# Performance work log

Measured on AMD Instinct MI355X. Metric: run time of the kernel, lower is better.

Reference implementation:

```python
import jax, jax.numpy as jnp
import numpy as np

N, E, FIN, H, C = 100000, 1600000, 128, 64, 40
EPS = 1e-5

def setup_inputs() -> dict:
    key = jax.random.key(0)
    ks = jax.random.split(key, 20)
    inp = {
        'x': jax.random.normal(ks[0], (N, FIN), jnp.float32),
        'edge_idx': jax.random.randint(ks[1], (2, E), 0, N, dtype=jnp.int64),
        'W1': jax.random.normal(ks[2], (FIN, H), jnp.float32) / np.sqrt(FIN),
        'b1': jnp.zeros((H,), jnp.float32),
        'g1': jnp.ones((H,), jnp.float32),
        'be1': jnp.zeros((H,), jnp.float32),
        'm1': jax.random.normal(ks[3], (H,), jnp.float32) * 0.1,
        'v1': jax.random.uniform(ks[4], (H,), jnp.float32) + 0.5,
        'W2': jax.random.normal(ks[5], (H, H), jnp.float32) / np.sqrt(H),
        'b2': jnp.zeros((H,), jnp.float32),
        'g2': jnp.ones((H,), jnp.float32),
        'be2': jnp.zeros((H,), jnp.float32),
        'm2': jax.random.normal(ks[6], (H,), jnp.float32) * 0.1,
        'v2': jax.random.uniform(ks[7], (H,), jnp.float32) + 0.5,
        'W3': jax.random.normal(ks[8], (H, C), jnp.float32) / np.sqrt(H),
        'b3': jnp.zeros((C,), jnp.float32),
    }
    return inp

def reference(x, edge_idx, W1, b1, g1, be1, m1, v1, W2, b2, g2, be2, m2, v2, W3, b3):
    n = x.shape[0]
    loop = jnp.arange(n, dtype=edge_idx.dtype)
    row = jnp.concatenate([edge_idx[0], loop])  # source nodes (+ self loops)
    col = jnp.concatenate([edge_idx[1], loop])  # target nodes (+ self loops)
    # symmetric gcn_norm: deg from unit edge weights aggregated at target
    deg = jax.ops.segment_sum(jnp.ones_like(row, dtype=x.dtype), col, num_segments=n)
    dinv = jnp.where(deg > 0, jax.lax.rsqrt(deg), 0.0)
    norm = dinv[row] * dinv[col]  # [E+N]

    def conv(h, W, b):
        hl = h @ W                            # dense transform first (PyG order)
        msg = hl[row] * norm[:, None]         # gather + edge scale
        agg = jax.ops.segment_sum(msg, col, num_segments=n)  # scatter-add
        return agg + b

    def bn(h, g, be, m, v):  # eval-mode BatchNorm1d (running stats)
        return g * (h - m) * jax.lax.rsqrt(v + EPS) + be

    h = jax.nn.relu(bn(conv(x, W1, b1), g1, be1, m1, v1))
    h = jax.nn.relu(bn(conv(h, W2, b2), g2, be2, m2, v2))
    return conv(h, W3, b3)
```

## Files before the change

### kernel.cpp

```cpp
#include <hip/hip_runtime.h>

#define EPSV 1e-5f
#define NB  1024
#define CAP 2048

typedef short short8 __attribute__((ext_vector_type(8)));
typedef float f32x4 __attribute__((ext_vector_type(4)));

__device__ inline unsigned short f2bf(float x) {
    unsigned u = __float_as_uint(x);
    unsigned r = (u + 0x7FFFu + ((u >> 16) & 1u)) >> 16;
    return (unsigned short)r;
}
__device__ inline float bf2f(unsigned short h) {
    return __uint_as_float(((unsigned)h) << 16);
}
__device__ inline float bflo(unsigned u) { return __uint_as_float(u << 16); }
__device__ inline float bfhi(unsigned u) { return __uint_as_float(u & 0xffff0000u); }
__device__ inline unsigned packbf(float x, float y) {
    return (unsigned)f2bf(x) | ((unsigned)f2bf(y) << 16);
}


__global__ __launch_bounds__(512) void k_bin(const int* __restrict__ row,
                                             const int* __restrict__ col,
                                             int* __restrict__ bcnt,
                                             unsigned* __restrict__ bkt,
                                             int E, int npb, int chunk) {
    __shared__ int hist[NB];
    __shared__ int fill[NB];
    const int tid = threadIdx.x;
    const int e0 = blockIdx.x * chunk;
    const int e1 = min(E, e0 + chunk);
    for (int j = tid; j < NB; j += 512) hist[j] = 0;
    __syncthreads();
    for (int i = e0 + tid; i < e1; i += 512)
        atomicAdd(&hist[col[i] / npb], 1);
    __syncthreads();
    for (int j = tid; j < NB; j += 512)
        fill[j] = hist[j] ? atomicAdd(&bcnt[j], hist[j]) : 0;
    __syncthreads();
    for (int i = e0 + tid; i < e1; i += 512) {
        const int c = col[i], r = row[i];
        const int b = c / npb;
        const int pos = atomicAdd(&fill[b], 1);
        if (pos < CAP)
            bkt[(size_t)b * CAP + pos] = ((unsigned)(c - b * npb) << 17) | (unsigned)r;
    }
}


__global__ __launch_bounds__(NB) void k_bscan(const int* __restrict__ bcnt,
                                              int* __restrict__ bbase,
                                              int* __restrict__ rowptr, int E, int n) {
    __shared__ int s[NB];
    const int t = threadIdx.x;
    const int v = min(bcnt[t], CAP);
    s[t] = v;
    __syncthreads();
    for (int off = 1; off < NB; off <<= 1) {
        int u = (t >= off) ? s[t - off] : 0;
        __syncthreads();
        s[t] += u;
        __syncthreads();
    }
    bbase[t] = s[t] - v;
    if (t == 0) rowptr[n] = E;
}


__global__ __launch_bounds__(256) void k_place(const int* __restrict__ bcnt,
                                               const int* __restrict__ bbase,
                                               const unsigned* __restrict__ bkt,
                                               int* __restrict__ rowptr,
                                               float* __restrict__ dinv,
                                               int* __restrict__ srcidx,
                                               int n, int npb) {
    __shared__ int hist[128];
    __shared__ int pfx[128];
    __shared__ unsigned ent[CAP];
    const int b = blockIdx.x;
    const int tid = threadIdx.x;
    const int c0 = b * npb;
    const int nn = min(npb, n - c0);
    if (nn <= 0) return;
    const int bc = min(bcnt[b], CAP);
    const int base = bbase[b];
    for (int j = tid; j < nn; j += 256) hist[j] = 0;
    __syncthreads();
    for (int i = tid; i < bc; i += 256) {
        const unsigned e = bkt[(size_t)b * CAP + i];
        ent[i] = e;
        atomicAdd(&hist[e >> 17], 1);
    }
    __syncthreads();
    if (tid == 0) {
        int run = base;
        for (int j = 0; j < nn; ++j) { pfx[j] = run; run += hist[j]; }
    }
    __syncthreads();
    for (int j = tid; j < nn; j += 256) {
        rowptr[c0 + j] = pfx[j];
        dinv[c0 + j] = rsqrtf((float)(hist[j] + 1));
    }
    __syncthreads();
    for (int i = tid; i < bc; i += 256) {
        const unsigned e = ent[i];
        const int pos = atomicAdd(&pfx[e >> 17], 1);
        srcidx[pos] = (int)(e & 0x1FFFFu);
    }
}


template<int K, int F, int NT>
__device__ inline void wprep_one(const float* __restrict__ W,
                                 unsigned short* __restrict__ out, int tid) {
    const int lane = tid & 63;
    const int nt = (tid >> 6) % NT;
    const int ks = tid / (64 * NT);
    const int col = nt * 16 + (lane & 15);
    const int k0 = ks * 32 + (lane >> 4) * 8;
    short8 h8, l8;
#pragma unroll
    for (int e = 0; e < 8; ++e) {
        const float w = (col < F) ? W[(size_t)(k0 + e) * F + col] : 0.f;
        const unsigned short h = f2bf(w);
        h8[e] = (short)h;
        l8[e] = (short)f2bf(w - bf2f(h));
    }
    short8* dst = (short8*)(out + (size_t)tid * 16);
    dst[0] = h8;
    dst[1] = l8;
}

__global__ __launch_bounds__(256) void k_wprep_all(const float* __restrict__ W1,
                                                   const float* __restrict__ W2,
                                                   const float* __restrict__ W3,
                                                   unsigned short* __restrict__ wf1,
                                                   unsigned short* __restrict__ wf2,
                                                   unsigned short* __restrict__ wf3) {
    const int tid = blockIdx.x * blockDim.x + threadIdx.x;
    if (tid < 1024) wprep_one<128, 64, 4>(W1, wf1, tid);
    else if (tid < 1536) wprep_one<64, 64, 4>(W2, wf2, tid - 1024);
    else if (tid < 1920) wprep_one<64, 40, 3>(W3, wf3, tid - 1536);
}


template<int K, int NT>
__global__ __launch_bounds__(256) void gemm_f32in(const float* __restrict__ X,
                                                  const unsigned short* __restrict__ wfrag,
                                                  const float* __restrict__ dinv,
                                                  unsigned* __restrict__ Y, int n) {
    const int lane = threadIdx.x & 63;
    const int wv = threadIdx.x >> 6;
    const int row0 = blockIdx.x * 64 + wv * 16;
    const int arow = row0 + (lane & 15);
    const bool aval = arow < n;

    f32x4 acc[NT];
#pragma unroll
    for (int t = 0; t < NT; ++t) acc[t] = (f32x4){0.f, 0.f, 0.f, 0.f};

#pragma unroll
    for (int ks = 0; ks < K / 32; ++ks) {
        float av[8];
        if (aval) {
            const float* ap = X + (size_t)arow * K + ks * 32 + (lane >> 4) * 8;
            const float4 p0 = *reinterpret_cast<const float4*>(ap);
            const float4 p1 = *reinterpret_cast<const float4*>(ap + 4);
            av[0] = p0.x; av[1] = p0.y; av[2] = p0.z; av[3] = p0.w;
            av[4] = p1.x; av[5] = p1.y; av[6] = p1.z; av[7] = p1.w;
        } else {
#pragma unroll
            for (int e = 0; e < 8; ++e) av[e] = 0.f;
        }
        short8 ah, al;
#pragma unroll
        for (int e = 0; e < 8; ++e) {
            const unsigned short h = f2bf(av[e]);
            ah[e] = (short)h;
            al[e] = (short)f2bf(av[e] - bf2f(h));
        }
#pragma unroll
        for (int t = 0; t < NT; ++t) {
            const short8* bp = (const short8*)(wfrag + (((size_t)ks * NT + t) * 64 + lane) * 16);
            const short8 bh = bp[0];
            const short8 bl = bp[1];
            acc[t] = __builtin_amdgcn_mfma_f32_16x16x32_bf16(ah, bh, acc[t], 0, 0, 0);
            acc[t] = __builtin_amdgcn_mfma_f32_16x16x32_bf16(al, bh, acc[t], 0, 0, 0);
            acc[t] = __builtin_amdgcn_mfma_f32_16x16x32_bf16(ah, bl, acc[t], 0, 0, 0);
        }
    }

    const int col = lane & 15;
    const int rg = lane >> 4;
#pragma unroll
    for (int r = 0; r < 4; ++r) {
        const int orow = row0 + rg * 4 + r;
        const float di = (orow < n) ? dinv[orow] : 0.f;
#pragma unroll
        for (int t = 0; t < NT; ++t) {
            const float val = acc[t][r] * di;
            const float oth = __shfl_xor(val, 1);
            if (!(lane & 1))
                Y[(size_t)orow * (NT * 8) + t * 8 + (col >> 1)] = packbf(val, oth);
        }
    }
}


template<int K, int NT, int MODE>
__global__ __launch_bounds__(256) void gemm_bf16in(const unsigned short* __restrict__ X,
                                                   const unsigned short* __restrict__ wfrag,
                                                   const float* __restrict__ dinv,
                                                   const float* __restrict__ bias,
                                                   void* __restrict__ Yv, int n) {
    const int lane = threadIdx.x & 63;
    const int wv = threadIdx.x >> 6;
    const int row0 = blockIdx.x * 64 + wv * 16;
    const int arow = row0 + (lane & 15);
    const bool aval = arow < n;

    f32x4 acc[NT];
#pragma unroll
    for (int t = 0; t < NT; ++t) acc[t] = (f32x4){0.f, 0.f, 0.f, 0.f};

#pragma unroll
    for (int ks = 0; ks < K / 32; ++ks) {
        short8 ah = {0, 0, 0, 0, 0, 0, 0, 0};
        if (aval)
            ah = *(const short8*)(X + (size_t)arow * K + ks * 32 + (lane >> 4) * 8);
#pragma unroll
        for (int t = 0; t < NT; ++t) {
            const short8* bp = (const short8*)(wfrag + (((size_t)ks * NT + t) * 64 + lane) * 16);
            const short8 bh = bp[0];
            const short8 bl = bp[1];
            acc[t] = __builtin_amdgcn_mfma_f32_16x16x32_bf16(ah, bh, acc[t], 0, 0, 0);
            acc[t] = __builtin_amdgcn_mfma_f32_16x16x32_bf16(ah, bl, acc[t], 0, 0, 0);
        }
    }

    const int col = lane & 15;
    const int rg = lane >> 4;
#pragma unroll
    for (int r = 0; r < 4; ++r) {
        const int orow = row0 + rg * 4 + r;
        if (MODE == 0) {
            const float di = (orow < n) ? dinv[orow] : 0.f;
            unsigned* Y = (unsigned*)Yv;
#pragma unroll
            for (int t = 0; t < NT; ++t) {
                const float val = acc[t][r] * di;
                const float oth = __shfl_xor(val, 1);
                if (!(lane & 1))
                    Y[(size_t)orow * (NT * 8) + t * 8 + (col >> 1)] = packbf(val, oth);
            }
        } else {
            float* Y = (float*)Yv;
#pragma unroll
            for (int t = 0; t < NT; ++t) {
                const int oc = t * 16 + col;
                if (orow < n && oc < 40)
                    Y[(size_t)orow * 40 + oc] = acc[t][r] + bias[oc];
            }
        }
    }
}


template<int MODE>
__global__ __launch_bounds__(256) void k_gather(const unsigned* __restrict__ in,
                                                const int* __restrict__ rowptr,
                                                const int* __restrict__ srcidx,
                                                const float* __restrict__ dinv,
                                                const float* __restrict__ b,
                                                const float* __restrict__ g,
                                                const float* __restrict__ be,
                                                const float* __restrict__ m,
                                                const float* __restrict__ v,
                                                unsigned* __restrict__ out, int n) {
    __shared__ unsigned offs[4][64];
    const int lane = threadIdx.x & 63;
    const int wslot = threadIdx.x >> 6;
    const int half = lane >> 5;
    const int p = lane & 31;
    const int node = blockIdx.x * 4 + wslot;

    if (node >= n) {
        if (!half) out[(size_t)node * 32 + p] = 0u;
        return;
    }

    const int s = rowptr[node], e = rowptr[node + 1];
    const unsigned pconst = (unsigned)p * 4u;
    const char* inb = (const char*)in;
    float ax = 0.f, ay = 0.f;

    for (int base = s; base < e; base += 64) {
        const int c = min(64, e - base);
        unsigned idx = (unsigned)n;
        if (base + lane < e) idx = (unsigned)srcidx[base + lane];
        offs[wslot][lane] = idx * 128u;
        for (int k8 = 0; k8 < 32; k8 += 8) {
            if (2 * k8 >= c) break;
            unsigned o[8], u[8];
#pragma unroll
            for (int j = 0; j < 8; ++j) o[j] = offs[wslot][2 * (k8 + j) + half];
#pragma unroll
            for (int j = 0; j < 8; ++j)
                u[j] = *(const unsigned*)(inb + (size_t)(o[j] + pconst));
#pragma unroll
            for (int j = 0; j < 8; ++j) { ax += bflo(u[j]); ay += bfhi(u[j]); }
        }
    }
    ax += __shfl_xor(ax, 32);
    ay += __shfl_xor(ay, 32);
    {
        const unsigned su = in[(size_t)node * 32 + p];
        ax += bflo(su); ay += bfhi(su);
    }
    const float di = dinv[node];
    float ox, oy;
    if (MODE == 2) {
        ox = ax * di; oy = ay * di;
    } else {
        const float2 bb = ((const float2*)b)[p];
        const float2 gg = ((const float2*)g)[p];
        const float2 bee = ((const float2*)be)[p];
        const float2 mm = ((const float2*)m)[p];
        const float2 vv = ((const float2*)v)[p];
        const float sx = gg.x * rsqrtf(vv.x + EPSV);
        const float sy = gg.y * rsqrtf(vv.y + EPSV);
        ox = fmaxf((ax * di + bb.x - mm.x) * sx + bee.x, 0.f);
        oy = fmaxf((ay * di + bb.y - mm.y) * sy + bee.y, 0.f);
        if (MODE == 1) { ox *= di; oy *= di; }
    }
    if (!half) out[(size_t)node * 32 + p] = packbf(ox, oy);
}


extern "C" void kernel_launch(void* const* d_in, const int* in_sizes, int n_in,
                              void* d_out, int out_size, void* d_ws, size_t ws_size,
                              hipStream_t stream) {
    const float* x   = (const float*)d_in[0];
    const int*   ei  = (const int*)d_in[1];
    const float* W1  = (const float*)d_in[2];
    const float* b1  = (const float*)d_in[3];
    const float* g1  = (const float*)d_in[4];
    const float* be1 = (const float*)d_in[5];
    const float* m1  = (const float*)d_in[6];
    const float* v1  = (const float*)d_in[7];
    const float* W2  = (const float*)d_in[8];
    const float* b2  = (const float*)d_in[9];
    const float* g2  = (const float*)d_in[10];
    const float* be2 = (const float*)d_in[11];
    const float* m2  = (const float*)d_in[12];
    const float* v2  = (const float*)d_in[13];
    const float* W3  = (const float*)d_in[14];
    const float* b3  = (const float*)d_in[15];

    const int n = in_sizes[0] / 128;
    const int E = in_sizes[1] / 2;
    const int* row  = ei;
    const int* colv = ei + E;
    const int npb = (n + NB - 1) / NB;
    const int gblk = (n >> 6) + 1;
    const int npad = gblk * 64;

    char* base = (char*)d_ws;
    size_t off = 0;
    auto alloc = [&](size_t bytes) -> char* {
        char* p = base + off;
        off += (bytes + 255) & ~(size_t)255;
        return p;
    };
    int*      bcnt   = (int*)     alloc((size_t)NB * 4);
    int*      bbase  = (int*)     alloc((size_t)NB * 4);
    unsigned* bkt    = (unsigned*)alloc((size_t)NB * CAP * 4);
    int*      rowptr = (int*)     alloc((size_t)(n + 1) * 4);
    int*      srcidx = (int*)     alloc((size_t)E * 4);
    float*    dinv   = (float*)   alloc((size_t)n * 4);
    unsigned* hls1u  = (unsigned*)alloc((size_t)npad * 32 * 4);
    unsigned* h1u    = (unsigned*)alloc((size_t)npad * 32 * 4);
    unsigned* hls2u  = (unsigned*)alloc((size_t)npad * 32 * 4);
    unsigned* h2lsu  = (unsigned*)alloc((size_t)npad * 32 * 4);
    unsigned* agg3u  = (unsigned*)alloc((size_t)npad * 32 * 4);
    unsigned short* wf1 = (unsigned short*)alloc((size_t)(128/32) * 4 * 64 * 32);
    unsigned short* wf2 = (unsigned short*)alloc((size_t)(64/32) * 4 * 64 * 32);
    unsigned short* wf3 = (unsigned short*)alloc((size_t)(64/32) * 3 * 64 * 32);
    float*    outp   = (float*)d_out;

    hipMemsetAsync(bcnt, 0, (size_t)NB * 4, stream);
    const int binblk = 128;
    const int chunk = (E + binblk - 1) / binblk;
    k_bin<<<binblk, 512, 0, stream>>>(row, colv, bcnt, bkt, E, npb, chunk);
    k_bscan<<<1, NB, 0, stream>>>(bcnt, bbase, rowptr, E, n);
    k_place<<<NB, 256, 0, stream>>>(bcnt, bbase, bkt, rowptr, dinv, srcidx, n, npb);

    k_wprep_all<<<8, 256, 0, stream>>>(W1, W2, W3, wf1, wf2, wf3);

    const int ablk = npad / 4;
    gemm_f32in<128, 4><<<gblk, 256, 0, stream>>>(x, wf1, dinv, hls1u, n);
    k_gather<0><<<ablk, 256, 0, stream>>>(hls1u, rowptr, srcidx, dinv,
                                          b1, g1, be1, m1, v1, h1u, n);
    gemm_bf16in<64, 4, 0><<<gblk, 256, 0, stream>>>((const unsigned short*)h1u, wf2,
                                                    dinv, nullptr, hls2u, n);
    k_gather<1><<<ablk, 256, 0, stream>>>(hls2u, rowptr, srcidx, dinv,
                                          b2, g2, be2, m2, v2, h2lsu, n);
    k_gather<2><<<ablk, 256, 0, stream>>>(h2lsu, rowptr, srcidx, dinv,
                                          nullptr, nullptr, nullptr, nullptr, nullptr,
                                          agg3u, n);
    gemm_bf16in<64, 3, 1><<<gblk, 256, 0, stream>>>((const unsigned short*)agg3u, wf3,
                                                    dinv, b3, outp, n);
}
```

Measured before the change: 209.2 us.

## Spread edge binning over many small blocks and keep edges in registers

```diff
diff --git a/kernel.cpp b/kernel.cpp
--- a/kernel.cpp
+++ b/kernel.cpp
@@ -3,6 +3,7 @@
 #define EPSV 1e-5f
 #define NB  1024
 #define CAP 2048
+#define BIN_ITER 4
 
 typedef short short8 __attribute__((ext_vector_type(8)));
 typedef float f32x4 __attribute__((ext_vector_type(4)));
@@ -22,30 +23,43 @@
 }
 
 
-__global__ __launch_bounds__(512) void k_bin(const int* __restrict__ row,
-                                             const int* __restrict__ col,
-                                             int* __restrict__ bcnt,
-                                             unsigned* __restrict__ bkt,
-                                             int E, int npb, int chunk) {
+__global__ __launch_bounds__(1024) void k_bin(const int* __restrict__ row,
+                                              const int* __restrict__ col,
+                                              int* __restrict__ bcnt,
+                                              unsigned* __restrict__ bkt,
+                                              int E, int npb) {
     __shared__ int hist[NB];
     __shared__ int fill[NB];
     const int tid = threadIdx.x;
-    const int e0 = blockIdx.x * chunk;
-    const int e1 = min(E, e0 + chunk);
-    for (int j = tid; j < NB; j += 512) hist[j] = 0;
-    __syncthreads();
-    for (int i = e0 + tid; i < e1; i += 512)
-        atomicAdd(&hist[col[i] / npb], 1);
-    __syncthreads();
-    for (int j = tid; j < NB; j += 512)
+    const int e0 = blockIdx.x * (1024 * BIN_ITER);
+    for (int j = tid; j < NB; j += 1024) hist[j] = 0;
+    __syncthreads();
+    unsigned ent[BIN_ITER];
+    int bb[BIN_ITER];
+#pragma unroll
+    for (int j = 0; j < BIN_ITER; ++j) {
+        const int i = e0 + j * 1024 + tid;
+        bb[j] = -1;
+        ent[j] = 0;
+        if (i < E) {
+            const int c = col[i], r = row[i];
+            const int b = c / npb;
+            bb[j] = b;
+            ent[j] = ((unsigned)(c - b * npb) << 17) | (unsigned)r;
+            atomicAdd(&hist[b], 1);
+        }
+    }
+    __syncthreads();
+    for (int j = tid; j < NB; j += 1024)
         fill[j] = hist[j] ? atomicAdd(&bcnt[j], hist[j]) : 0;
     __syncthreads();
-    for (int i = e0 + tid; i < e1; i += 512) {
-        const int c = col[i], r = row[i];
-        const int b = c / npb;
-        const int pos = atomicAdd(&fill[b], 1);
-        if (pos < CAP)
-            bkt[(size_t)b * CAP + pos] = ((unsigned)(c - b * npb) << 17) | (unsigned)r;
+#pragma unroll
+    for (int j = 0; j < BIN_ITER; ++j) {
+        if (bb[j] >= 0) {
+            const int pos = atomicAdd(&fill[bb[j]], 1);
+            if (pos < CAP)
+                bkt[(size_t)bb[j] * CAP + pos] = ent[j];
+        }
     }
 }
 
@@ -391,9 +405,8 @@
     float*    outp   = (float*)d_out;
 
     hipMemsetAsync(bcnt, 0, (size_t)NB * 4, stream);
-    const int binblk = 128;
-    const int chunk = (E + binblk - 1) / binblk;
-    k_bin<<<binblk, 512, 0, stream>>>(row, colv, bcnt, bkt, E, npb, chunk);
+    const int binblk = (E + 1024 * BIN_ITER - 1) / (1024 * BIN_ITER);
+    k_bin<<<binblk, 1024, 0, stream>>>(row, colv, bcnt, bkt, E, npb);
     k_bscan<<<1, NB, 0, stream>>>(bcnt, bbase, rowptr, E, n);
     k_place<<<NB, 256, 0, stream>>>(bcnt, bbase, bkt, rowptr, dinv, srcidx, n, npb);
 
```

After: 196.0 us. -6.3%, faster.
